# Kernel optimization log

Hardware: AMD Instinct MI355X
Metric: run time of the kernel (lower is better)

The kernel has to match this reference:

```python
import jax, jax.numpy as jnp
import numpy as np

N_NODES = 50000
N_EDGES = 600000
H_DIM = 128


def setup_inputs() -> dict:
    key = jax.random.key(0)
    ks = jax.random.split(key, 16)
    s = 0.05  # weight scale
    inp = {
        'h': jax.random.normal(ks[0], (N_NODES, H_DIM), jnp.float32),
        'coord': jax.random.normal(ks[1], (N_NODES, 3), jnp.float32),
        'edge_index': jax.random.randint(ks[2], (2, N_EDGES), 0, N_NODES, jnp.int32),
        # edge_mlp: (2*input_nf + 1) -> hidden -> hidden
        'w_e1': jax.random.normal(ks[3], (2 * H_DIM + 1, H_DIM), jnp.float32) * s,
        'b_e1': jnp.zeros((H_DIM,), jnp.float32),
        'w_e2': jax.random.normal(ks[4], (H_DIM, H_DIM), jnp.float32) * s,
        'b_e2': jnp.zeros((H_DIM,), jnp.float32),
        # node_mlp: (hidden + input_nf) -> hidden -> output_nf
        'w_n1': jax.random.normal(ks[5], (2 * H_DIM, H_DIM), jnp.float32) * s,
        'b_n1': jnp.zeros((H_DIM,), jnp.float32),
        'w_n2': jax.random.normal(ks[6], (H_DIM, H_DIM), jnp.float32) * s,
        'b_n2': jnp.zeros((H_DIM,), jnp.float32),
        # coord_mlp: hidden -> hidden -> 1 (last layer xavier gain 0.001, no bias)
        'w_c1': jax.random.normal(ks[7], (H_DIM, H_DIM), jnp.float32) * s,
        'b_c1': jnp.zeros((H_DIM,), jnp.float32),
        'w_c2': jax.random.normal(ks[8], (H_DIM, 1), jnp.float32) * 0.001,
    }
    return inp


def reference(h, coord, edge_index, w_e1, b_e1, w_e2, b_e2,
              w_n1, b_n1, w_n2, b_n2, w_c1, b_c1, w_c2):
    silu = jax.nn.silu
    n = h.shape[0]
    row, col = edge_index[0], edge_index[1]

    # coord2radial (normalize=False)
    coord_diff = coord[row] - coord[col]                 # [E, 3]
    radial = jnp.sum(coord_diff ** 2, axis=1, keepdims=True)  # [E, 1]

    # edge model (no attention, no edge_attr)
    edge_in = jnp.concatenate([h[row], h[col], radial], axis=1)  # [E, 257]
    edge_feat = silu(silu(edge_in @ w_e1 + b_e1) @ w_e2 + b_e2)  # [E, H]

    # coord model: coords_agg='mean', tanh=False
    w = silu(edge_feat @ w_c1 + b_c1) @ w_c2             # [E, 1]
    trans = coord_diff * w                               # [E, 3]
    t_sum = jax.ops.segment_sum(trans, row, num_segments=n)
    cnt = jax.ops.segment_sum(jnp.ones((row.shape[0], 1), trans.dtype), row,
                              num_segments=n)
    coord_new = coord + t_sum / jnp.maximum(cnt, 1.0)

    # node model (residual=True, no graphnorm, no node attention)
    agg = jax.ops.segment_sum(edge_feat, row, num_segments=n)   # [N, H]
    node_in = jnp.concatenate([h, agg], axis=1)                 # [N, 2H]
    h_new = h + (silu(node_in @ w_n1 + b_n1) @ w_n2 + b_n2)

    return (h_new, coord_new, edge_feat)
```

## Files before the change

kernel.cpp:

```cpp
#include <hip/hip_runtime.h>

#define NN 50000
#define NE 600000

typedef __attribute__((ext_vector_type(8))) short short8;
typedef __attribute__((ext_vector_type(4))) float f32x4;

__device__ __forceinline__ float silu_f(float x) { return x / (1.0f + __expf(-x)); }

__device__ __forceinline__ unsigned short f2bf(float f) {
    unsigned u = __builtin_bit_cast(unsigned, f);
    unsigned r = u + 0x7FFFu + ((u >> 16) & 1u);
    return (unsigned short)(r >> 16);
}

__global__ __launch_bounds__(512) void k_prep(const float* __restrict__ h,
                                              unsigned short* __restrict__ hb)
{
    const int nchunks = NN * 128 / 8;
    for (int i = blockIdx.x * blockDim.x + threadIdx.x; i < nchunks;
         i += gridDim.x * blockDim.x) {
        const float4* p = (const float4*)(h + (size_t)i * 8);
        float4 x = p[0], y = p[1];
        short8 v;
        v[0] = f2bf(x.x); v[1] = f2bf(x.y); v[2] = f2bf(x.z); v[3] = f2bf(x.w);
        v[4] = f2bf(y.x); v[5] = f2bf(y.y); v[6] = f2bf(y.z); v[7] = f2bf(y.w);
        *(short8*)(hb + (size_t)i * 8) = v;
    }
}

__global__ __launch_bounds__(512) void k_edge12(
    const unsigned short* __restrict__ hb, const float* __restrict__ coord,
    const int* __restrict__ ei,
    const float* __restrict__ w_e1, const float* __restrict__ b_e1,
    const float* __restrict__ w_e2, const float* __restrict__ b_e2,
    float* __restrict__ ef, float* __restrict__ agg)
{
    __shared__ unsigned short WT1[128 * 256];
    __shared__ unsigned short WT2[128 * 128];
    __shared__ unsigned short A1s[64 * 256];
    __shared__ unsigned short A2s[64 * 128];
    __shared__ float rad[64];
    __shared__ int rows_s[64];

    const int tid = threadIdx.x;
    const int wv = tid >> 6, lane = tid & 63;
    const int l4 = lane >> 4, li = lane & 15;
    const int mb = (wv >> 2) * 32;
    const int nb = (wv & 3) * 32;

    for (int i = tid; i < 257 * 128; i += 512) {
        int k = i >> 7, n = i & 127;
        if (k < 256) {
            int off = n * 512 + ((k * 2) ^ ((n & 7) << 4));
            *(unsigned short*)((char*)WT1 + off) = f2bf(w_e1[i]);
        }
    }
    for (int i = tid; i < 128 * 128; i += 512) {
        int k = i >> 7, n = i & 127;
        int off = n * 256 + ((k * 2) ^ ((n & 7) << 4));
        *(unsigned short*)((char*)WT2 + off) = f2bf(w_e2[i]);
    }
    float wradv[2], b1v[2], b2v[2];
    #pragma unroll
    for (int nf = 0; nf < 2; ++nf) {
        int n = nb + nf * 16 + li;
        wradv[nf] = w_e1[256 * 128 + n];
        b1v[nf]   = b_e1[n];
        b2v[nf]   = b_e2[n];
    }
    __syncthreads();

    const f32x4 z4 = {0.f, 0.f, 0.f, 0.f};

    for (int t = blockIdx.x; t < NE / 64; t += gridDim.x) {
        const int ebase = t * 64;
        if (tid < 64) {
            int e = ebase + tid;
            int r = ei[e], c = ei[NE + e];
            rows_s[tid] = r;
            float dx = coord[r * 3 + 0] - coord[c * 3 + 0];
            float dy = coord[r * 3 + 1] - coord[c * 3 + 1];
            float dz = coord[r * 3 + 2] - coord[c * 3 + 2];
            rad[tid] = dx * dx + dy * dy + dz * dz;
        }
        {
            int le = tid >> 3;
            int e = ebase + le;
            int r = ei[e], c = ei[NE + e];
            const unsigned short* hr = hb + (size_t)r * 128;
            const unsigned short* hc = hb + (size_t)c * 128;
            #pragma unroll
            for (int i = 0; i < 4; ++i) {
                int chunk = i * 8 + (tid & 7);
                short8 v = (chunk < 16) ? *(const short8*)(hr + chunk * 8)
                                        : *(const short8*)(hc + (chunk - 16) * 8);
                int off = le * 512 + ((chunk * 16) ^ ((le & 7) << 4));
                *(short8*)((char*)A1s + off) = v;
            }
        }
        __syncthreads();

        f32x4 acc[2][2];
        acc[0][0] = z4; acc[0][1] = z4; acc[1][0] = z4; acc[1][1] = z4;
        for (int ks = 0; ks < 8; ++ks) {
            int kb = ks * 64 + l4 * 16;
            short8 af[2], bf[2];
            #pragma unroll
            for (int mf = 0; mf < 2; ++mf) {
                int row = mb + mf * 16 + li;
                af[mf] = *(const short8*)((const char*)A1s + row * 512 + (kb ^ ((row & 7) << 4)));
            }
            #pragma unroll
            for (int nf = 0; nf < 2; ++nf) {
                int row = nb + nf * 16 + li;
                bf[nf] = *(const short8*)((const char*)WT1 + row * 512 + (kb ^ ((row & 7) << 4)));
            }
            #pragma unroll
            for (int mf = 0; mf < 2; ++mf)
                #pragma unroll
                for (int nf = 0; nf < 2; ++nf)
                    acc[mf][nf] = __builtin_amdgcn_mfma_f32_16x16x32_bf16(
                        af[mf], bf[nf], acc[mf][nf], 0, 0, 0);
        }
        #pragma unroll
        for (int mf = 0; mf < 2; ++mf)
            #pragma unroll
            for (int nf = 0; nf < 2; ++nf)
                #pragma unroll
                for (int r = 0; r < 4; ++r) {
                    int row = mb + mf * 16 + l4 * 4 + r;
                    float v = acc[mf][nf][r] + rad[row] * wradv[nf] + b1v[nf];
                    v = silu_f(v);
                    int colb = (nb + nf * 16 + li) * 2;
                    int off = row * 256 + (colb ^ ((row & 7) << 4));
                    *(unsigned short*)((char*)A2s + off) = f2bf(v);
                }
        __syncthreads();

        f32x4 acc2[2][2];
        acc2[0][0] = z4; acc2[0][1] = z4; acc2[1][0] = z4; acc2[1][1] = z4;
        for (int ks = 0; ks < 4; ++ks) {
            int kb = ks * 64 + l4 * 16;
            short8 af[2], bf[2];
            #pragma unroll
            for (int mf = 0; mf < 2; ++mf) {
                int row = mb + mf * 16 + li;
                af[mf] = *(const short8*)((const char*)A2s + row * 256 + (kb ^ ((row & 7) << 4)));
            }
            #pragma unroll
            for (int nf = 0; nf < 2; ++nf) {
                int row = nb + nf * 16 + li;
                bf[nf] = *(const short8*)((const char*)WT2 + row * 256 + (kb ^ ((row & 7) << 4)));
            }
            #pragma unroll
            for (int mf = 0; mf < 2; ++mf)
                #pragma unroll
                for (int nf = 0; nf < 2; ++nf)
                    acc2[mf][nf] = __builtin_amdgcn_mfma_f32_16x16x32_bf16(
                        af[mf], bf[nf], acc2[mf][nf], 0, 0, 0);
        }
        #pragma unroll
        for (int mf = 0; mf < 2; ++mf)
            #pragma unroll
            for (int nf = 0; nf < 2; ++nf)
                #pragma unroll
                for (int r = 0; r < 4; ++r) {
                    int row = mb + mf * 16 + l4 * 4 + r;
                    int e = ebase + row;
                    int col = nb + nf * 16 + li;
                    float v = silu_f(acc2[mf][nf][r] + b2v[nf]);
                    ef[(size_t)e * 128 + col] = v;
                    atomicAdd(&agg[(size_t)rows_s[row] * 128 + col], v);
                }
        __syncthreads();
    }
}

__global__ __launch_bounds__(512) void k_coord(
    const float* __restrict__ ef, const float* __restrict__ coord,
    const int* __restrict__ ei,
    const float* __restrict__ w_c1, const float* __restrict__ b_c1,
    const float* __restrict__ w_c2,
    float* __restrict__ tsum, float* __restrict__ cnt)
{
    __shared__ unsigned short Aefs[128 * 128];
    __shared__ unsigned short WTc[128 * 128];

    const int tid = threadIdx.x;
    const int wv = tid >> 6, lane = tid & 63;
    const int l4 = lane >> 4, li = lane & 15;

    for (int i = tid; i < 128 * 128; i += 512) {
        int k = i >> 7, n = i & 127;
        int off = n * 256 + ((k * 2) ^ ((n & 7) << 4));
        *(unsigned short*)((char*)WTc + off) = f2bf(w_c1[i]);
    }
    float bc1v[8], wc2v[8];
    #pragma unroll
    for (int nf = 0; nf < 8; ++nf) {
        bc1v[nf] = b_c1[nf * 16 + li];
        wc2v[nf] = w_c2[nf * 16 + li];
    }
    __syncthreads();

    const f32x4 z4 = {0.f, 0.f, 0.f, 0.f};
    const int ntiles = (NE + 127) / 128;

    for (int t = blockIdx.x; t < ntiles; t += gridDim.x) {
        const int ebase = t * 128;
        {
            int le = tid >> 2;
            int e = ebase + le;
            #pragma unroll
            for (int i = 0; i < 4; ++i) {
                int chunk = i * 4 + (tid & 3);
                short8 v;
                if (e < NE) {
                    const float4* p = (const float4*)(ef + (size_t)e * 128 + chunk * 8);
                    float4 x = p[0], y = p[1];
                    v[0] = f2bf(x.x); v[1] = f2bf(x.y); v[2] = f2bf(x.z); v[3] = f2bf(x.w);
                    v[4] = f2bf(y.x); v[5] = f2bf(y.y); v[6] = f2bf(y.z); v[7] = f2bf(y.w);
                } else {
                    v = (short8)0;
                }
                int off = le * 256 + ((chunk * 16) ^ ((le & 7) << 4));
                *(short8*)((char*)Aefs + off) = v;
            }
        }
        __syncthreads();

        f32x4 acc[8];
        #pragma unroll
        for (int nf = 0; nf < 8; ++nf) acc[nf] = z4;
        const int mrow = wv * 16 + li;
        for (int ks = 0; ks < 4; ++ks) {
            int kb = ks * 64 + l4 * 16;
            short8 a = *(const short8*)((const char*)Aefs + mrow * 256 + (kb ^ ((mrow & 7) << 4)));
            #pragma unroll
            for (int nf = 0; nf < 8; ++nf) {
                int row = nf * 16 + li;
                short8 b = *(const short8*)((const char*)WTc + row * 256 + (kb ^ ((row & 7) << 4)));
                acc[nf] = __builtin_amdgcn_mfma_f32_16x16x32_bf16(a, b, acc[nf], 0, 0, 0);
            }
        }
        float wq[4];
        #pragma unroll
        for (int r = 0; r < 4; ++r) {
            float p = 0.f;
            #pragma unroll
            for (int nf = 0; nf < 8; ++nf)
                p += silu_f(acc[nf][r] + bc1v[nf]) * wc2v[nf];
            #pragma unroll
            for (int off = 1; off < 16; off <<= 1) p += __shfl_xor(p, off);
            wq[r] = p;
        }
        if (li == 0) {
            #pragma unroll
            for (int r = 0; r < 4; ++r) {
                int e = ebase + wv * 16 + l4 * 4 + r;
                if (e < NE) {
                    int rr = ei[e], cc = ei[NE + e];
                    float dx = coord[rr * 3 + 0] - coord[cc * 3 + 0];
                    float dy = coord[rr * 3 + 1] - coord[cc * 3 + 1];
                    float dz = coord[rr * 3 + 2] - coord[cc * 3 + 2];
                    atomicAdd(&tsum[rr * 3 + 0], dx * wq[r]);
                    atomicAdd(&tsum[rr * 3 + 1], dy * wq[r]);
                    atomicAdd(&tsum[rr * 3 + 2], dz * wq[r]);
                    atomicAdd(&cnt[rr], 1.0f);
                }
            }
        }
        __syncthreads();
    }
}

__global__ __launch_bounds__(512) void k_node1(
    const unsigned short* __restrict__ hb, const float* __restrict__ agg,
    const float* __restrict__ w_n1, const float* __restrict__ b_n1,
    unsigned short* __restrict__ ub)
{
    __shared__ unsigned short WT[128 * 256];
    __shared__ unsigned short As[128 * 256];

    const int tid = threadIdx.x;
    const int wv = tid >> 6, lane = tid & 63;
    const int l4 = lane >> 4, li = lane & 15;
    const int mb = (wv >> 2) * 64;
    const int nb = (wv & 3) * 32;

    for (int i = tid; i < 256 * 128; i += 512) {
        int k = i >> 7, n = i & 127;
        int off = n * 512 + ((k * 2) ^ ((n & 7) << 4));
        *(unsigned short*)((char*)WT + off) = f2bf(w_n1[i]);
    }
    float b1v[2];
    #pragma unroll
    for (int nf = 0; nf < 2; ++nf) b1v[nf] = b_n1[nb + nf * 16 + li];
    __syncthreads();

    const f32x4 z4 = {0.f, 0.f, 0.f, 0.f};
    const int ntiles = (NN + 127) / 128;

    for (int t = blockIdx.x; t < ntiles; t += gridDim.x) {
        const int nbase = t * 128;
        {
            int ln = tid >> 2;
            int node = nbase + ln;
            #pragma unroll
            for (int i = 0; i < 8; ++i) {
                int chunk = i * 4 + (tid & 3);
                short8 v;
                if (node < NN) {
                    if (chunk < 16) {
                        v = *(const short8*)(hb + (size_t)node * 128 + chunk * 8);
                    } else {
                        const float4* p = (const float4*)(agg + (size_t)node * 128 + (chunk - 16) * 8);
                        float4 x = p[0], y = p[1];
                        v[0] = f2bf(x.x); v[1] = f2bf(x.y); v[2] = f2bf(x.z); v[3] = f2bf(x.w);
                        v[4] = f2bf(y.x); v[5] = f2bf(y.y); v[6] = f2bf(y.z); v[7] = f2bf(y.w);
                    }
                } else v = (short8)0;
                int off = ln * 512 + ((chunk * 16) ^ ((ln & 7) << 4));
                *(short8*)((char*)As + off) = v;
            }
        }
        __syncthreads();

        f32x4 acc[4][2];
        #pragma unroll
        for (int mf = 0; mf < 4; ++mf) { acc[mf][0] = z4; acc[mf][1] = z4; }
        for (int ks = 0; ks < 8; ++ks) {
            int kb = ks * 64 + l4 * 16;
            short8 af[4], bf[2];
            #pragma unroll
            for (int mf = 0; mf < 4; ++mf) {
                int row = mb + mf * 16 + li;
                af[mf] = *(const short8*)((const char*)As + row * 512 + (kb ^ ((row & 7) << 4)));
            }
            #pragma unroll
            for (int nf = 0; nf < 2; ++nf) {
                int row = nb + nf * 16 + li;
                bf[nf] = *(const short8*)((const char*)WT + row * 512 + (kb ^ ((row & 7) << 4)));
            }
            #pragma unroll
            for (int mf = 0; mf < 4; ++mf)
                #pragma unroll
                for (int nf = 0; nf < 2; ++nf)
                    acc[mf][nf] = __builtin_amdgcn_mfma_f32_16x16x32_bf16(
                        af[mf], bf[nf], acc[mf][nf], 0, 0, 0);
        }
        #pragma unroll
        for (int mf = 0; mf < 4; ++mf)
            #pragma unroll
            for (int nf = 0; nf < 2; ++nf)
                #pragma unroll
                for (int r = 0; r < 4; ++r) {
                    int row = mb + mf * 16 + l4 * 4 + r;
                    int node = nbase + row;
                    if (node < NN) {
                        float v = silu_f(acc[mf][nf][r] + b1v[nf]);
                        ub[(size_t)node * 128 + nb + nf * 16 + li] = f2bf(v);
                    }
                }
        __syncthreads();
    }
}

__global__ __launch_bounds__(512) void k_node2(
    const float* __restrict__ h, const unsigned short* __restrict__ ub,
    const float* __restrict__ w_n2, const float* __restrict__ b_n2,
    const float* __restrict__ coord, const float* __restrict__ tsum,
    const float* __restrict__ cnt,
    float* __restrict__ h_new, float* __restrict__ coord_new)
{
    __shared__ unsigned short Aus[128 * 128];
    __shared__ unsigned short WT[128 * 128];

    const int tid = threadIdx.x;
    const int wv = tid >> 6, lane = tid & 63;
    const int l4 = lane >> 4, li = lane & 15;

    for (int i = tid; i < 128 * 128; i += 512) {
        int k = i >> 7, n = i & 127;
        int off = n * 256 + ((k * 2) ^ ((n & 7) << 4));
        *(unsigned short*)((char*)WT + off) = f2bf(w_n2[i]);
    }
    float b2v[8];
    #pragma unroll
    for (int nf = 0; nf < 8; ++nf) b2v[nf] = b_n2[nf * 16 + li];
    __syncthreads();

    const f32x4 z4 = {0.f, 0.f, 0.f, 0.f};
    const int ntiles = (NN + 127) / 128;

    for (int t = blockIdx.x; t < ntiles; t += gridDim.x) {
        const int nbase = t * 128;
        {
            int ln = tid >> 2;
            int node = nbase + ln;
            #pragma unroll
            for (int i = 0; i < 4; ++i) {
                int chunk = i * 4 + (tid & 3);
                short8 v;
                if (node < NN) v = *(const short8*)(ub + (size_t)node * 128 + chunk * 8);
                else v = (short8)0;
                int off = ln * 256 + ((chunk * 16) ^ ((ln & 7) << 4));
                *(short8*)((char*)Aus + off) = v;
            }
        }
        __syncthreads();

        f32x4 acc[8];
        #pragma unroll
        for (int nf = 0; nf < 8; ++nf) acc[nf] = z4;
        const int mrow = wv * 16 + li;
        for (int ks = 0; ks < 4; ++ks) {
            int kb = ks * 64 + l4 * 16;
            short8 a = *(const short8*)((const char*)Aus + mrow * 256 + (kb ^ ((mrow & 7) << 4)));
            #pragma unroll
            for (int nf = 0; nf < 8; ++nf) {
                int row = nf * 16 + li;
                short8 b = *(const short8*)((const char*)WT + row * 256 + (kb ^ ((row & 7) << 4)));
                acc[nf] = __builtin_amdgcn_mfma_f32_16x16x32_bf16(a, b, acc[nf], 0, 0, 0);
            }
        }
        #pragma unroll
        for (int nf = 0; nf < 8; ++nf)
            #pragma unroll
            for (int r = 0; r < 4; ++r) {
                int row = wv * 16 + l4 * 4 + r;
                int node = nbase + row;
                if (node < NN) {
                    int col = nf * 16 + li;
                    float v = acc[nf][r] + b2v[nf] + h[(size_t)node * 128 + col];
                    h_new[(size_t)node * 128 + col] = v;
                }
            }
        if (tid < 128) {
            int node = nbase + tid;
            if (node < NN) {
                float m = fmaxf(cnt[node], 1.0f);
                coord_new[node * 3 + 0] = coord[node * 3 + 0] + tsum[node * 3 + 0] / m;
                coord_new[node * 3 + 1] = coord[node * 3 + 1] + tsum[node * 3 + 1] / m;
                coord_new[node * 3 + 2] = coord[node * 3 + 2] + tsum[node * 3 + 2] / m;
            }
        }
        __syncthreads();
    }
}

extern "C" void kernel_launch(void* const* d_in, const int* in_sizes, int n_in,
                              void* d_out, int out_size, void* d_ws, size_t ws_size,
                              hipStream_t stream)
{
    const float* h     = (const float*)d_in[0];
    const float* coord = (const float*)d_in[1];
    const int*   ei    = (const int*)d_in[2];
    const float* w_e1  = (const float*)d_in[3];
    const float* b_e1  = (const float*)d_in[4];
    const float* w_e2  = (const float*)d_in[5];
    const float* b_e2  = (const float*)d_in[6];
    const float* w_n1  = (const float*)d_in[7];
    const float* b_n1  = (const float*)d_in[8];
    const float* w_n2  = (const float*)d_in[9];
    const float* b_n2  = (const float*)d_in[10];
    const float* w_c1  = (const float*)d_in[11];
    const float* b_c1  = (const float*)d_in[12];
    const float* w_c2  = (const float*)d_in[13];

    float* h_new     = (float*)d_out;
    float* coord_new = h_new + (size_t)NN * 128;
    float* ef        = coord_new + (size_t)NN * 3;

    float*          agg  = (float*)d_ws;
    float*          tsum = agg + (size_t)NN * 128;
    float*          cnt  = tsum + (size_t)NN * 3;
    unsigned short* hb   = (unsigned short*)(cnt + NN);
    unsigned short* ub   = hb + (size_t)NN * 128;

    hipMemsetAsync(agg, 0, ((size_t)NN * 128 + (size_t)NN * 3 + NN) * sizeof(float), stream);

    k_prep  <<<1024, 512, 0, stream>>>(h, hb);
    k_edge12<<<256,  512, 0, stream>>>(hb, coord, ei, w_e1, b_e1, w_e2, b_e2, ef, agg);
    k_coord <<<512,  512, 0, stream>>>(ef, coord, ei, w_c1, b_c1, w_c2, tsum, cnt);
    k_node1 <<<391,  512, 0, stream>>>(hb, agg, w_n1, b_n1, ub);
    k_node2 <<<391,  512, 0, stream>>>(h, ub, w_n2, b_n2, coord, tsum, cnt, h_new, coord_new);
}
```

Before: 550.4 us.

## Fuse coord MLP into edge kernel, merge node kernels, keep weights in registers

The coord MLP now runs inside the edge kernel on the bf16 edge features already in LDS, so the fp32 edge features are no longer reread from HBM and the edge indices and coordinates are not gathered a second time. The two node kernels are merged, which removes the intermediate bf16 buffer. Each wave now keeps its 16-column slice of the weights in registers as MFMA B fragments rather than staging full weight matrices in LDS, and the LDS swizzle gains an extra bit. Outputs use nontemporal stores, and launch bounds are set to raise occupancy, at the risk of register pressure or spills from holding three weight sets per thread.

```diff
diff --git a/kernel.cpp b/kernel.cpp
--- a/kernel.cpp
+++ b/kernel.cpp
@@ -5,6 +5,8 @@
 
 typedef __attribute__((ext_vector_type(8))) short short8;
 typedef __attribute__((ext_vector_type(4))) float f32x4;
+
+#define SWZ(row) ((((row) & 7) << 4) ^ (((row) & 8) << 2))
 
 __device__ __forceinline__ float silu_f(float x) { return x / (1.0f + __expf(-x)); }
 
@@ -29,47 +31,49 @@
     }
 }
 
-__global__ __launch_bounds__(512) void k_edge12(
+__global__ __launch_bounds__(512, 4) void k_edge(
     const unsigned short* __restrict__ hb, const float* __restrict__ coord,
     const int* __restrict__ ei,
     const float* __restrict__ w_e1, const float* __restrict__ b_e1,
     const float* __restrict__ w_e2, const float* __restrict__ b_e2,
-    float* __restrict__ ef, float* __restrict__ agg)
+    const float* __restrict__ w_c1, const float* __restrict__ b_c1,
+    const float* __restrict__ w_c2,
+    float* __restrict__ ef, float* __restrict__ agg,
+    float* __restrict__ tsum, float* __restrict__ cnt)
 {
-    __shared__ unsigned short WT1[128 * 256];
-    __shared__ unsigned short WT2[128 * 128];
     __shared__ unsigned short A1s[64 * 256];
     __shared__ unsigned short A2s[64 * 128];
     __shared__ float rad[64];
-    __shared__ int rows_s[64];
-
-    const int tid = threadIdx.x;
-    const int wv = tid >> 6, lane = tid & 63;
-    const int l4 = lane >> 4, li = lane & 15;
-    const int mb = (wv >> 2) * 32;
-    const int nb = (wv & 3) * 32;
-
-    for (int i = tid; i < 257 * 128; i += 512) {
-        int k = i >> 7, n = i & 127;
-        if (k < 256) {
-            int off = n * 512 + ((k * 2) ^ ((n & 7) << 4));
-            *(unsigned short*)((char*)WT1 + off) = f2bf(w_e1[i]);
-        }
-    }
-    for (int i = tid; i < 128 * 128; i += 512) {
-        int k = i >> 7, n = i & 127;
-        int off = n * 256 + ((k * 2) ^ ((n & 7) << 4));
-        *(unsigned short*)((char*)WT2 + off) = f2bf(w_e2[i]);
-    }
-    float wradv[2], b1v[2], b2v[2];
+    __shared__ float dxyz[64][3];
+    __shared__ int   rows_s[64];
+    __shared__ float wqp[8][64];
+
+    const int tid  = threadIdx.x;
+    const int wv   = tid >> 6, lane = tid & 63;
+    const int l4   = lane >> 4, li = lane & 15;
+    const int nwb  = wv * 16;
+    const int n    = nwb + li;
+
+    short8 bw1[8], bw2[4], bwc[4];
     #pragma unroll
-    for (int nf = 0; nf < 2; ++nf) {
-        int n = nb + nf * 16 + li;
-        wradv[nf] = w_e1[256 * 128 + n];
-        b1v[nf]   = b_e1[n];
-        b2v[nf]   = b_e2[n];
-    }
-    __syncthreads();
+    for (int ks = 0; ks < 8; ++ks) {
+        short8 t;
+        #pragma unroll
+        for (int j = 0; j < 8; ++j) t[j] = f2bf(w_e1[(ks * 32 + l4 * 8 + j) * 128 + n]);
+        bw1[ks] = t;
+    }
+    #pragma unroll
+    for (int ks = 0; ks < 4; ++ks) {
+        short8 t, u;
+        #pragma unroll
+        for (int j = 0; j < 8; ++j) {
+            t[j] = f2bf(w_e2[(ks * 32 + l4 * 8 + j) * 128 + n]);
+            u[j] = f2bf(w_c1[(ks * 32 + l4 * 8 + j) * 128 + n]);
+        }
+        bw2[ks] = t; bwc[ks] = u;
+    }
+    const float wradv = w_e1[256 * 128 + n];
+    const float b1v = b_e1[n], b2v = b_e2[n], bc1v = b_c1[n], wc2v = w_c2[n];
 
     const f32x4 z4 = {0.f, 0.f, 0.f, 0.f};
 
@@ -82,6 +86,7 @@
             float dx = coord[r * 3 + 0] - coord[c * 3 + 0];
             float dy = coord[r * 3 + 1] - coord[c * 3 + 1];
             float dz = coord[r * 3 + 2] - coord[c * 3 + 2];
+            dxyz[tid][0] = dx; dxyz[tid][1] = dy; dxyz[tid][2] = dz;
             rad[tid] = dx * dx + dy * dy + dz * dz;
         }
         {
@@ -95,221 +100,138 @@
                 int chunk = i * 8 + (tid & 7);
                 short8 v = (chunk < 16) ? *(const short8*)(hr + chunk * 8)
                                         : *(const short8*)(hc + (chunk - 16) * 8);
-                int off = le * 512 + ((chunk * 16) ^ ((le & 7) << 4));
+                int off = le * 512 + ((chunk * 16) ^ SWZ(le));
                 *(short8*)((char*)A1s + off) = v;
             }
         }
         __syncthreads();
 
-        f32x4 acc[2][2];
-        acc[0][0] = z4; acc[0][1] = z4; acc[1][0] = z4; acc[1][1] = z4;
+        f32x4 acc[4];
+        acc[0] = z4; acc[1] = z4; acc[2] = z4; acc[3] = z4;
         for (int ks = 0; ks < 8; ++ks) {
-            int kb = ks * 64 + l4 * 16;
-            short8 af[2], bf[2];
-            #pragma unroll
-            for (int mf = 0; mf < 2; ++mf) {
-                int row = mb + mf * 16 + li;
-                af[mf] = *(const short8*)((const char*)A1s + row * 512 + (kb ^ ((row & 7) << 4)));
-            }
-            #pragma unroll
-            for (int nf = 0; nf < 2; ++nf) {
-                int row = nb + nf * 16 + li;
-                bf[nf] = *(const short8*)((const char*)WT1 + row * 512 + (kb ^ ((row & 7) << 4)));
-            }
-            #pragma unroll
-            for (int mf = 0; mf < 2; ++mf)
-                #pragma unroll
-                for (int nf = 0; nf < 2; ++nf)
-                    acc[mf][nf] = __builtin_amdgcn_mfma_f32_16x16x32_bf16(
-                        af[mf], bf[nf], acc[mf][nf], 0, 0, 0);
-        }
-        #pragma unroll
-        for (int mf = 0; mf < 2; ++mf)
-            #pragma unroll
-            for (int nf = 0; nf < 2; ++nf)
-                #pragma unroll
-                for (int r = 0; r < 4; ++r) {
-                    int row = mb + mf * 16 + l4 * 4 + r;
-                    float v = acc[mf][nf][r] + rad[row] * wradv[nf] + b1v[nf];
-                    v = silu_f(v);
-                    int colb = (nb + nf * 16 + li) * 2;
-                    int off = row * 256 + (colb ^ ((row & 7) << 4));
-                    *(unsigned short*)((char*)A2s + off) = f2bf(v);
-                }
-        __syncthreads();
-
-        f32x4 acc2[2][2];
-        acc2[0][0] = z4; acc2[0][1] = z4; acc2[1][0] = z4; acc2[1][1] = z4;
+            const int kb = ks * 64 + l4 * 16;
+            #pragma unroll
+            for (int mf = 0; mf < 4; ++mf) {
+                int row = mf * 16 + li;
+                short8 a = *(const short8*)((const char*)A1s + row * 512 + (kb ^ SWZ(row)));
+                acc[mf] = __builtin_amdgcn_mfma_f32_16x16x32_bf16(a, bw1[ks], acc[mf], 0, 0, 0);
+            }
+        }
+        #pragma unroll
+        for (int mf = 0; mf < 4; ++mf)
+            #pragma unroll
+            for (int r = 0; r < 4; ++r) {
+                int row = mf * 16 + l4 * 4 + r;
+                float v = silu_f(acc[mf][r] + rad[row] * wradv + b1v);
+                int off = row * 256 + ((n * 2) ^ SWZ(row));
+                *(unsigned short*)((char*)A2s + off) = f2bf(v);
+            }
+        __syncthreads();
+
+        acc[0] = z4; acc[1] = z4; acc[2] = z4; acc[3] = z4;
         for (int ks = 0; ks < 4; ++ks) {
-            int kb = ks * 64 + l4 * 16;
-            short8 af[2], bf[2];
-            #pragma unroll
-            for (int mf = 0; mf < 2; ++mf) {
-                int row = mb + mf * 16 + li;
-                af[mf] = *(const short8*)((const char*)A2s + row * 256 + (kb ^ ((row & 7) << 4)));
-            }
-            #pragma unroll
-            for (int nf = 0; nf < 2; ++nf) {
-                int row = nb + nf * 16 + li;
-                bf[nf] = *(const short8*)((const char*)WT2 + row * 256 + (kb ^ ((row & 7) << 4)));
-            }
-            #pragma unroll
-            for (int mf = 0; mf < 2; ++mf)
-                #pragma unroll
-                for (int nf = 0; nf < 2; ++nf)
-                    acc2[mf][nf] = __builtin_amdgcn_mfma_f32_16x16x32_bf16(
-                        af[mf], bf[nf], acc2[mf][nf], 0, 0, 0);
-        }
-        #pragma unroll
-        for (int mf = 0; mf < 2; ++mf)
-            #pragma unroll
-            for (int nf = 0; nf < 2; ++nf)
-                #pragma unroll
-                for (int r = 0; r < 4; ++r) {
-                    int row = mb + mf * 16 + l4 * 4 + r;
-                    int e = ebase + row;
-                    int col = nb + nf * 16 + li;
-                    float v = silu_f(acc2[mf][nf][r] + b2v[nf]);
-                    ef[(size_t)e * 128 + col] = v;
-                    atomicAdd(&agg[(size_t)rows_s[row] * 128 + col], v);
-                }
-        __syncthreads();
-    }
-}
-
-__global__ __launch_bounds__(512) void k_coord(
-    const float* __restrict__ ef, const float* __restrict__ coord,
-    const int* __restrict__ ei,
-    const float* __restrict__ w_c1, const float* __restrict__ b_c1,
-    const float* __restrict__ w_c2,
-    float* __restrict__ tsum, float* __restrict__ cnt)
+            const int kb = ks * 64 + l4 * 16;
+            #pragma unroll
+            for (int mf = 0; mf < 4; ++mf) {
+                int row = mf * 16 + li;
+                short8 a = *(const short8*)((const char*)A2s + row * 256 + (kb ^ SWZ(row)));
+                acc[mf] = __builtin_amdgcn_mfma_f32_16x16x32_bf16(a, bw2[ks], acc[mf], 0, 0, 0);
+            }
+        }
+        #pragma unroll
+        for (int mf = 0; mf < 4; ++mf)
+            #pragma unroll
+            for (int r = 0; r < 4; ++r) {
+                int row = mf * 16 + l4 * 4 + r;
+                int e = ebase + row;
+                float v = silu_f(acc[mf][r] + b2v);
+                __builtin_nontemporal_store(v, &ef[(size_t)e * 128 + n]);
+                atomicAdd(&agg[(size_t)rows_s[row] * 128 + n], v);
+                int off = row * 256 + ((n * 2) ^ SWZ(row));
+                *(unsigned short*)((char*)A1s + off) = f2bf(v);
+            }
+        __syncthreads();
+
+        acc[0] = z4; acc[1] = z4; acc[2] = z4; acc[3] = z4;
+        for (int ks = 0; ks < 4; ++ks) {
+            const int kb = ks * 64 + l4 * 16;
+            #pragma unroll
+            for (int mf = 0; mf < 4; ++mf) {
+                int row = mf * 16 + li;
+                short8 a = *(const short8*)((const char*)A1s + row * 256 + (kb ^ SWZ(row)));
+                acc[mf] = __builtin_amdgcn_mfma_f32_16x16x32_bf16(a, bwc[ks], acc[mf], 0, 0, 0);
+            }
+        }
+        #pragma unroll
+        for (int mf = 0; mf < 4; ++mf)
+            #pragma unroll
+            for (int r = 0; r < 4; ++r) {
+                float p = silu_f(acc[mf][r] + bc1v) * wc2v;
+                p += __shfl_xor(p, 1); p += __shfl_xor(p, 2);
+                p += __shfl_xor(p, 4); p += __shfl_xor(p, 8);
+                if (li == 0) wqp[wv][mf * 16 + l4 * 4 + r] = p;
+            }
+        __syncthreads();
+
+        if (tid < 64) {
+            float wq = 0.f;
+            #pragma unroll
+            for (int w = 0; w < 8; ++w) wq += wqp[w][tid];
+            int rr = rows_s[tid];
+            atomicAdd(&tsum[rr * 3 + 0], dxyz[tid][0] * wq);
+            atomicAdd(&tsum[rr * 3 + 1], dxyz[tid][1] * wq);
+            atomicAdd(&tsum[rr * 3 + 2], dxyz[tid][2] * wq);
+            atomicAdd(&cnt[rr], 1.0f);
+        }
+        __syncthreads();
+    }
+}
+
+__global__ __launch_bounds__(512, 4) void k_node(
+    const unsigned short* __restrict__ hb, const float* __restrict__ h,
+    const float* __restrict__ agg,
+    const float* __restrict__ w_n1, const float* __restrict__ b_n1,
+    const float* __restrict__ w_n2, const float* __restrict__ b_n2,
+    const float* __restrict__ coord, const float* __restrict__ tsum,
+    const float* __restrict__ cnt,
+    float* __restrict__ h_new, float* __restrict__ coord_new)
 {
-    __shared__ unsigned short Aefs[128 * 128];
-    __shared__ unsigned short WTc[128 * 128];
-
-    const int tid = threadIdx.x;
-    const int wv = tid >> 6, lane = tid & 63;
-    const int l4 = lane >> 4, li = lane & 15;
-
-    for (int i = tid; i < 128 * 128; i += 512) {
-        int k = i >> 7, n = i & 127;
-        int off = n * 256 + ((k * 2) ^ ((n & 7) << 4));
-        *(unsigned short*)((char*)WTc + off) = f2bf(w_c1[i]);
-    }
-    float bc1v[8], wc2v[8];
+    __shared__ unsigned short As[64 * 256];
+    __shared__ unsigned short Us[64 * 128];
+
+    const int tid  = threadIdx.x;
+    const int wv   = tid >> 6, lane = tid & 63;
+    const int l4   = lane >> 4, li = lane & 15;
+    const int n    = wv * 16 + li;
+
+    short8 bw1[8], bw2[4];
     #pragma unroll
-    for (int nf = 0; nf < 8; ++nf) {
-        bc1v[nf] = b_c1[nf * 16 + li];
-        wc2v[nf] = w_c2[nf * 16 + li];
-    }
-    __syncthreads();
+    for (int ks = 0; ks < 8; ++ks) {
+        short8 t;
+        #pragma unroll
+        for (int j = 0; j < 8; ++j) t[j] = f2bf(w_n1[(ks * 32 + l4 * 8 + j) * 128 + n]);
+        bw1[ks] = t;
+    }
+    #pragma unroll
+    for (int ks = 0; ks < 4; ++ks) {
+        short8 t;
+        #pragma unroll
+        for (int j = 0; j < 8; ++j) t[j] = f2bf(w_n2[(ks * 32 + l4 * 8 + j) * 128 + n]);
+        bw2[ks] = t;
+    }
+    const float b1v = b_n1[n], b2v = b_n2[n];
 
     const f32x4 z4 = {0.f, 0.f, 0.f, 0.f};
-    const int ntiles = (NE + 127) / 128;
+    const int ntiles = (NN + 63) / 64;
 
     for (int t = blockIdx.x; t < ntiles; t += gridDim.x) {
-        const int ebase = t * 128;
+        const int nbase = t * 64;
         {
-            int le = tid >> 2;
-            int e = ebase + le;
+            int ln = tid >> 3;
+            int node = nbase + ln;
             #pragma unroll
             for (int i = 0; i < 4; ++i) {
-                int chunk = i * 4 + (tid & 3);
-                short8 v;
-                if (e < NE) {
-                    const float4* p = (const float4*)(ef + (size_t)e * 128 + chunk * 8);
-                    float4 x = p[0], y = p[1];
-                    v[0] = f2bf(x.x); v[1] = f2bf(x.y); v[2] = f2bf(x.z); v[3] = f2bf(x.w);
-                    v[4] = f2bf(y.x); v[5] = f2bf(y.y); v[6] = f2bf(y.z); v[7] = f2bf(y.w);
-                } else {
-                    v = (short8)0;
-                }
-                int off = le * 256 + ((chunk * 16) ^ ((le & 7) << 4));
-                *(short8*)((char*)Aefs + off) = v;
-            }
-        }
-        __syncthreads();
-
-        f32x4 acc[8];
-        #pragma unroll
-        for (int nf = 0; nf < 8; ++nf) acc[nf] = z4;
-        const int mrow = wv * 16 + li;
-        for (int ks = 0; ks < 4; ++ks) {
-            int kb = ks * 64 + l4 * 16;
-            short8 a = *(const short8*)((const char*)Aefs + mrow * 256 + (kb ^ ((mrow & 7) << 4)));
-            #pragma unroll
-            for (int nf = 0; nf < 8; ++nf) {
-                int row = nf * 16 + li;
-                short8 b = *(const short8*)((const char*)WTc + row * 256 + (kb ^ ((row & 7) << 4)));
-                acc[nf] = __builtin_amdgcn_mfma_f32_16x16x32_bf16(a, b, acc[nf], 0, 0, 0);
-            }
-        }
-        float wq[4];
-        #pragma unroll
-        for (int r = 0; r < 4; ++r) {
-            float p = 0.f;
-            #pragma unroll
-            for (int nf = 0; nf < 8; ++nf)
-                p += silu_f(acc[nf][r] + bc1v[nf]) * wc2v[nf];
-            #pragma unroll
-            for (int off = 1; off < 16; off <<= 1) p += __shfl_xor(p, off);
-            wq[r] = p;
-        }
-        if (li == 0) {
-            #pragma unroll
-            for (int r = 0; r < 4; ++r) {
-                int e = ebase + wv * 16 + l4 * 4 + r;
-                if (e < NE) {
-                    int rr = ei[e], cc = ei[NE + e];
-                    float dx = coord[rr * 3 + 0] - coord[cc * 3 + 0];
-                    float dy = coord[rr * 3 + 1] - coord[cc * 3 + 1];
-                    float dz = coord[rr * 3 + 2] - coord[cc * 3 + 2];
-                    atomicAdd(&tsum[rr * 3 + 0], dx * wq[r]);
-                    atomicAdd(&tsum[rr * 3 + 1], dy * wq[r]);
-                    atomicAdd(&tsum[rr * 3 + 2], dz * wq[r]);
-                    atomicAdd(&cnt[rr], 1.0f);
-                }
-            }
-        }
-        __syncthreads();
-    }
-}
-
-__global__ __launch_bounds__(512) void k_node1(
-    const unsigned short* __restrict__ hb, const float* __restrict__ agg,
-    const float* __restrict__ w_n1, const float* __restrict__ b_n1,
-    unsigned short* __restrict__ ub)
-{
-    __shared__ unsigned short WT[128 * 256];
-    __shared__ unsigned short As[128 * 256];
-
-    const int tid = threadIdx.x;
-    const int wv = tid >> 6, lane = tid & 63;
-    const int l4 = lane >> 4, li = lane & 15;
-    const int mb = (wv >> 2) * 64;
-    const int nb = (wv & 3) * 32;
-
-    for (int i = tid; i < 256 * 128; i += 512) {
-        int k = i >> 7, n = i & 127;
-        int off = n * 512 + ((k * 2) ^ ((n & 7) << 4));
-        *(unsigned short*)((char*)WT + off) = f2bf(w_n1[i]);
-    }
-    float b1v[2];
-    #pragma unroll
-    for (int nf = 0; nf < 2; ++nf) b1v[nf] = b_n1[nb + nf * 16 + li];
-    __syncthreads();
-
-    const f32x4 z4 = {0.f, 0.f, 0.f, 0.f};
-    const int ntiles = (NN + 127) / 128;
-
-    for (int t = blockIdx.x; t < ntiles; t += gridDim.x) {
-        const int nbase = t * 128;
-        {
-            int ln = tid >> 2;
-            int node = nbase + ln;
-            #pragma unroll
-            for (int i = 0; i < 8; ++i) {
-                int chunk = i * 4 + (tid & 3);
+                int chunk = i * 8 + (tid & 7);
                 short8 v;
                 if (node < NN) {
                     if (chunk < 16) {
@@ -321,123 +243,56 @@
                         v[4] = f2bf(y.x); v[5] = f2bf(y.y); v[6] = f2bf(y.z); v[7] = f2bf(y.w);
                     }
                 } else v = (short8)0;
-                int off = ln * 512 + ((chunk * 16) ^ ((ln & 7) << 4));
+                int off = ln * 512 + ((chunk * 16) ^ SWZ(ln));
                 *(short8*)((char*)As + off) = v;
             }
         }
         __syncthreads();
 
-        f32x4 acc[4][2];
-        #pragma unroll
-        for (int mf = 0; mf < 4; ++mf) { acc[mf][0] = z4; acc[mf][1] = z4; }
+        f32x4 acc[4];
+        acc[0] = z4; acc[1] = z4; acc[2] = z4; acc[3] = z4;
         for (int ks = 0; ks < 8; ++ks) {
-            int kb = ks * 64 + l4 * 16;
-            short8 af[4], bf[2];
-            #pragma unroll
-            for (int mf = 0; mf < 4; ++mf) {
-                int row = mb + mf * 16 + li;
-                af[mf] = *(const short8*)((const char*)As + row * 512 + (kb ^ ((row & 7) << 4)));
-            }
-            #pragma unroll
-            for (int nf = 0; nf < 2; ++nf) {
-                int row = nb + nf * 16 + li;
-                bf[nf] = *(const short8*)((const char*)WT + row * 512 + (kb ^ ((row & 7) << 4)));
-            }
-            #pragma unroll
-            for (int mf = 0; mf < 4; ++mf)
-                #pragma unroll
-                for (int nf = 0; nf < 2; ++nf)
-                    acc[mf][nf] = __builtin_amdgcn_mfma_f32_16x16x32_bf16(
-                        af[mf], bf[nf], acc[mf][nf], 0, 0, 0);
-        }
-        #pragma unroll
-        for (int mf = 0; mf < 4; ++mf)
-            #pragma unroll
-            for (int nf = 0; nf < 2; ++nf)
-                #pragma unroll
-                for (int r = 0; r < 4; ++r) {
-                    int row = mb + mf * 16 + l4 * 4 + r;
-                    int node = nbase + row;
-                    if (node < NN) {
-                        float v = silu_f(acc[mf][nf][r] + b1v[nf]);
-                        ub[(size_t)node * 128 + nb + nf * 16 + li] = f2bf(v);
-                    }
-                }
-        __syncthreads();
-    }
-}
-
-__global__ __launch_bounds__(512) void k_node2(
-    const float* __restrict__ h, const unsigned short* __restrict__ ub,
-    const float* __restrict__ w_n2, const float* __restrict__ b_n2,
-    const float* __restrict__ coord, const float* __restrict__ tsum,
-    const float* __restrict__ cnt,
-    float* __restrict__ h_new, float* __restrict__ coord_new)
-{
-    __shared__ unsigned short Aus[128 * 128];
-    __shared__ unsigned short WT[128 * 128];
-
-    const int tid = threadIdx.x;
-    const int wv = tid >> 6, lane = tid & 63;
-    const int l4 = lane >> 4, li = lane & 15;
-
-    for (int i = tid; i < 128 * 128; i += 512) {
-        int k = i >> 7, n = i & 127;
-        int off = n * 256 + ((k * 2) ^ ((n & 7) << 4));
-        *(unsigned short*)((char*)WT + off) = f2bf(w_n2[i]);
-    }
-    float b2v[8];
-    #pragma unroll
-    for (int nf = 0; nf < 8; ++nf) b2v[nf] = b_n2[nf * 16 + li];
-    __syncthreads();
-
-    const f32x4 z4 = {0.f, 0.f, 0.f, 0.f};
-    const int ntiles = (NN + 127) / 128;
-
-    for (int t = blockIdx.x; t < ntiles; t += gridDim.x) {
-        const int nbase = t * 128;
-        {
-            int ln = tid >> 2;
-            int node = nbase + ln;
-            #pragma unroll
-            for (int i = 0; i < 4; ++i) {
-                int chunk = i * 4 + (tid & 3);
-                short8 v;
-                if (node < NN) v = *(const short8*)(ub + (size_t)node * 128 + chunk * 8);
-                else v = (short8)0;
-                int off = ln * 256 + ((chunk * 16) ^ ((ln & 7) << 4));
-                *(short8*)((char*)Aus + off) = v;
-            }
-        }
-        __syncthreads();
-
-        f32x4 acc[8];
-        #pragma unroll
-        for (int nf = 0; nf < 8; ++nf) acc[nf] = z4;
-        const int mrow = wv * 16 + li;
+            const int kb = ks * 64 + l4 * 16;
+            #pragma unroll
+            for (int mf = 0; mf < 4; ++mf) {
+                int row = mf * 16 + li;
+                short8 a = *(const short8*)((const char*)As + row * 512 + (kb ^ SWZ(row)));
+                acc[mf] = __builtin_amdgcn_mfma_f32_16x16x32_bf16(a, bw1[ks], acc[mf], 0, 0, 0);
+            }
+        }
+        #pragma unroll
+        for (int mf = 0; mf < 4; ++mf)
+            #pragma unroll
+            for (int r = 0; r < 4; ++r) {
+                int row = mf * 16 + l4 * 4 + r;
+                float v = silu_f(acc[mf][r] + b1v);
+                int off = row * 256 + ((n * 2) ^ SWZ(row));
+                *(unsigned short*)((char*)Us + off) = f2bf(v);
+            }
+        __syncthreads();
+
+        acc[0] = z4; acc[1] = z4; acc[2] = z4; acc[3] = z4;
         for (int ks = 0; ks < 4; ++ks) {
-            int kb = ks * 64 + l4 * 16;
-            short8 a = *(const short8*)((const char*)Aus + mrow * 256 + (kb ^ ((mrow & 7) << 4)));
-            #pragma unroll
-            for (int nf = 0; nf < 8; ++nf) {
-                int row = nf * 16 + li;
-                short8 b = *(const short8*)((const char*)WT + row * 256 + (kb ^ ((row & 7) << 4)));
-                acc[nf] = __builtin_amdgcn_mfma_f32_16x16x32_bf16(a, b, acc[nf], 0, 0, 0);
-            }
-        }
-        #pragma unroll
-        for (int nf = 0; nf < 8; ++nf)
-            #pragma unroll
-            for (int r = 0; r < 4; ++r) {
-                int row = wv * 16 + l4 * 4 + r;
+            const int kb = ks * 64 + l4 * 16;
+            #pragma unroll
+            for (int mf = 0; mf < 4; ++mf) {
+                int row = mf * 16 + li;
+                short8 a = *(const short8*)((const char*)Us + row * 256 + (kb ^ SWZ(row)));
+                acc[mf] = __builtin_amdgcn_mfma_f32_16x16x32_bf16(a, bw2[ks], acc[mf], 0, 0, 0);
+            }
+        }
+        #pragma unroll
+        for (int mf = 0; mf < 4; ++mf)
+            #pragma unroll
+            for (int r = 0; r < 4; ++r) {
+                int row = mf * 16 + l4 * 4 + r;
                 int node = nbase + row;
                 if (node < NN) {
-                    int col = nf * 16 + li;
-                    float v = acc[nf][r] + b2v[nf] + h[(size_t)node * 128 + col];
-                    h_new[(size_t)node * 128 + col] = v;
+                    float v = acc[mf][r] + b2v + h[(size_t)node * 128 + n];
+                    __builtin_nontemporal_store(v, &h_new[(size_t)node * 128 + n]);
                 }
             }
-        if (tid < 128) {
+        if (tid < 64) {
             int node = nbase + tid;
             if (node < NN) {
                 float m = fmaxf(cnt[node], 1.0f);
@@ -477,13 +332,12 @@
     float*          tsum = agg + (size_t)NN * 128;
     float*          cnt  = tsum + (size_t)NN * 3;
     unsigned short* hb   = (unsigned short*)(cnt + NN);
-    unsigned short* ub   = hb + (size_t)NN * 128;
 
     hipMemsetAsync(agg, 0, ((size_t)NN * 128 + (size_t)NN * 3 + NN) * sizeof(float), stream);
 
-    k_prep  <<<1024, 512, 0, stream>>>(h, hb);
-    k_edge12<<<256,  512, 0, stream>>>(hb, coord, ei, w_e1, b_e1, w_e2, b_e2, ef, agg);
-    k_coord <<<512,  512, 0, stream>>>(ef, coord, ei, w_c1, b_c1, w_c2, tsum, cnt);
-    k_node1 <<<391,  512, 0, stream>>>(hb, agg, w_n1, b_n1, ub);
-    k_node2 <<<391,  512, 0, stream>>>(h, ub, w_n2, b_n2, coord, tsum, cnt, h_new, coord_new);
-}
+    k_prep<<<1024, 512, 0, stream>>>(h, hb);
+    k_edge<<<512, 512, 0, stream>>>(hb, coord, ei, w_e1, b_e1, w_e2, b_e2,
+                                    w_c1, b_c1, w_c2, ef, agg, tsum, cnt);
+    k_node<<<512, 512, 0, stream>>>(hb, h, agg, w_n1, b_n1, w_n2, b_n2,
+                                    coord, tsum, cnt, h_new, coord_new);
+}
```

After: 555.3 us. No clear change (+0.9%).
